# Kernel tuning notes

Hardware: AMD Instinct MI355X
Metric: run time of the kernel (lower is better)

Reference implementation:

```python
import jax, jax.numpy as jnp
import numpy as np

IN_DIM, UNITS, OUT_DIM = 128, 256, 8
DENSITY = 0.5  # 1 - sparsity_level
B, T = 256, 512


def _ncp_dims():
    Nm = OUT_DIM
    Nc = max(int(0.4 * (UNITS - Nm)), 1)   # command neurons (AutoNCP rule)
    Ni = UNITS - Nm - Nc                    # inter neurons
    return Ni, Nc, Nm


def _fanout_mask(rng, n_src, n_dst, fanout):
    # each source connects to `fanout` distinct random destinations
    idx = np.argsort(rng.random((n_src, n_dst)), axis=1)[:, :fanout]
    m = np.zeros((n_src, n_dst), dtype=np.int32)
    m[np.arange(n_src)[:, None], idx] = 1
    return m


def setup_inputs() -> dict:
    key = jax.random.key(0)
    rng = np.random.default_rng(22222)
    Ni, Nc, Nm = _ncp_dims()
    s_fan = max(int(Ni * DENSITY), 1)       # sensory fanout
    i_fan = max(int(Nc * DENSITY), 1)       # inter fanout
    m_fanin = max(int(Nc * DENSITY), 1)     # motor fanin
    M_si = _fanout_mask(rng, IN_DIM, Ni, s_fan)      # sensory -> inter
    M_ic = _fanout_mask(rng, Ni, Nc, i_fan)          # inter -> command
    M_cm = _fanout_mask(rng, Nm, Nc, m_fanin).T      # command -> motor (fanin per motor)

    def layer_mask(M_in, hid):
        # WiredCfCCell: concat input sparsity with dense ones for the recurrent block, then transpose
        return np.concatenate([M_in, np.ones((hid, hid), np.int32)], axis=0).T

    masks = [layer_mask(M_si, Ni), layer_mask(M_ic, Nc), layer_mask(M_cm, Nm)]
    dims = [(IN_DIM, Ni), (Ni, Nc), (Nc, Nm)]
    inp = {}
    for l, (fin, hid) in enumerate(dims):
        cat = fin + hid
        scale = 1.0 / np.sqrt(cat)
        for nm in ("w1", "w2", "wa", "wb"):
            inp[f"{nm}_{l}"] = jnp.asarray(rng.normal(0.0, scale, (hid, cat)).astype(np.float32))
        for nm in ("b1", "b2", "ba", "bb"):
            inp[f"{nm}_{l}"] = jnp.zeros((hid,), jnp.float32)
        inp[f"m{l}"] = jnp.asarray(masks[l])  # int32, constant sparsity mask
    k1, k2 = jax.random.split(key)
    inp["x"] = jax.random.normal(k1, (B, T, IN_DIM), jnp.float32)
    inp["dt"] = jax.random.uniform(k2, (1,), jnp.float32, 0.5, 1.5)
    return inp


def _cfc_cell(xh, w1, b1, w2, b2, wa, ba, wb, bb, m, ts):
    # CfCCell, mode='default', no backbone, sparsity mask on ff1/ff2 weights
    mf = m.astype(w1.dtype)
    ff1 = jnp.tanh(xh @ (w1 * mf).T + b1)
    ff2 = jnp.tanh(xh @ (w2 * mf).T + b2)
    t_interp = jax.nn.sigmoid((xh @ wa.T + ba) * ts + (xh @ wb.T + bb))
    return ff1 * (1.0 - t_interp) + t_interp * ff2


def _forward(x, dt, params, masks):
    Ni, Nc, Nm = _ncp_dims()
    ts = dt[0]
    h0 = jnp.zeros((x.shape[0], Ni), x.dtype)
    h1 = jnp.zeros((x.shape[0], Nc), x.dtype)
    h2 = jnp.zeros((x.shape[0], Nm), x.dtype)
    p0, p1, p2 = params

    def step(carry, xt):
        h0, h1, h2 = carry
        nh0 = _cfc_cell(jnp.concatenate([xt, h0], 1), *p0, masks[0], ts)
        nh1 = _cfc_cell(jnp.concatenate([nh0, h1], 1), *p1, masks[1], ts)
        nh2 = _cfc_cell(jnp.concatenate([nh1, h2], 1), *p2, masks[2], ts)
        return (nh0, nh1, nh2), nh2

    (h0, h1, h2), ys = jax.lax.scan(step, (h0, h1, h2), jnp.swapaxes(x, 0, 1))
    y = jnp.tanh(jnp.swapaxes(ys, 0, 1))          # (B, T, OUT_DIM), tanh output saturation
    h_out = jnp.concatenate([h0, h1, h2], axis=1)  # (B, units)
    return y, h_out


def reference(x, dt,
              w1_0, b1_0, w2_0, b2_0, wa_0, ba_0, wb_0, bb_0, m0,
              w1_1, b1_1, w2_1, b2_1, wa_1, ba_1, wb_1, bb_1, m1,
              w1_2, b1_2, w2_2, b2_2, wa_2, ba_2, wb_2, bb_2, m2):
    params = ((w1_0, b1_0, w2_0, b2_0, wa_0, ba_0, wb_0, bb_0),
              (w1_1, b1_1, w2_1, b2_1, wa_1, ba_1, wb_1, bb_1),
              (w1_2, b1_2, w2_2, b2_2, wa_2, ba_2, wb_2, bb_2))
    return _forward(x, dt, params, (m0, m1, m2))
```

## Files before the change

kernel.cpp:

```cpp
#include <hip/hip_runtime.h>
#include <cmath>


typedef _Float16 f16;
typedef f16 h4 __attribute__((ext_vector_type(4)));
typedef f16 h8 __attribute__((ext_vector_type(8)));
typedef float f4 __attribute__((ext_vector_type(4)));

#define MFMA(a, b, c) __builtin_amdgcn_mfma_f32_16x16x32_f16(a, b, c, 0, 0, 0)
#define RAW_BAR() asm volatile("s_waitcnt lgkmcnt(0)\n\ts_barrier" ::: "memory")

constexpr int IN_DIM = 128, Ni = 149, Nc = 99, Nm = 8;
constexpr int CAT0 = 277, CAT1 = 248, CAT2 = 107;
constexpr int Bsz = 256, Tsz = 512;
constexpr int TC = 64, NCH = 8, NBT = 16;
constexpr int NT0 = 30, NT1 = 21;
constexpr int S0 = 168, S2 = 136;
constexpr int NXWG1 = 64;
constexpr int NXWG0 = 128;
constexpr size_t XU0C = (size_t)TC * NBT * NT0 * 256;
constexpr size_t NH0C = (size_t)TC * NBT * 2560;
constexpr size_t XU1C = (size_t)TC * NBT * NT1 * 256;
constexpr size_t H0S_HALVES = (size_t)NBT * 16 * S0;
constexpr size_t H12S_HALVES = (size_t)NBT * 2 * 16 * S2;
constexpr size_t YOFF = (size_t)Bsz * Tsz * 8;

constexpr int OFF_X0 = 0;
constexpr int OFF_R0 = 7680;
constexpr int OFF_X1 = 17280;
constexpr int OFF_R12A = 24000;
constexpr int OFF_R12B = 29376;
constexpr int NFRAG = 30144;

__device__ inline float rcpf_(float x) { return __builtin_amdgcn_rcpf(x); }
__device__ __forceinline__ float cfc_h(float a0, float a1, float a2) {
  float e0 = __expf(a0), e1 = __expf(a1), e2 = __expf(a2);
  float pa = 1.f + e0, ma = 1.f - e0;
  float pb = 1.f + e1, mb = 1.f - e1;
  float pc = 1.f + e2;
  float num = fmaf(ma * pb, e2, mb * pa);
  return num * rcpf_(pa * pb * pc);
}
__device__ __forceinline__ float tanhp_(float x) {
  float e = __expf(-2.f * x);
  return (1.f - e) * rcpf_(1.f + e);
}

__global__ __launch_bounds__(256) void pack_kernel(
    const float* __restrict__ w1_0, const float* __restrict__ w2_0,
    const float* __restrict__ wa_0, const float* __restrict__ wb_0,
    const int* __restrict__ m0,
    const float* __restrict__ w1_1, const float* __restrict__ w2_1,
    const float* __restrict__ wa_1, const float* __restrict__ wb_1,
    const int* __restrict__ m1,
    const float* __restrict__ w1_2, const float* __restrict__ w2_2,
    const float* __restrict__ wa_2, const float* __restrict__ wb_2,
    const int* __restrict__ m2, const float* __restrict__ dtp,
    f16* __restrict__ PK) {
  int idx = blockIdx.x * 256 + threadIdx.x;
  if (idx >= NFRAG) return;
  int lane = idx & 63, col = lane & 15, q = lane >> 4;
  float ts = dtp[0];
  const float* Wa = nullptr;
  const float* Wb = nullptr;
  const int* M = nullptr;
  int ld, n, nmax, k0, kmax;
  int mat;
  if (idx < OFF_R0) {
    int p = idx >> 6;
    mat = p / 40; int nt = (p >> 2) % 10, kt = p & 3;
    ld = CAT0; n = nt * 16 + col; nmax = Ni; k0 = kt * 32 + q * 8; kmax = IN_DIM;
    if (mat == 0) { Wa = w1_0; M = m0; }
    else if (mat == 1) { Wa = w2_0; M = m0; }
    else { Wa = wa_0; Wb = wb_0; }
  } else if (idx < OFF_X1) {
    int p = (idx - OFF_R0) >> 6;
    int g = p / 15; mat = (p / 5) % 3; int kt = p % 5;
    ld = CAT0; n = g * 16 + col; nmax = Ni; k0 = IN_DIM + kt * 32 + q * 8; kmax = CAT0;
    if (mat == 0) Wa = w1_0;
    else if (mat == 1) Wa = w2_0;
    else { Wa = wa_0; Wb = wb_0; }
  } else if (idx < OFF_R12A) {
    int p = (idx - OFF_X1) >> 6;
    mat = p / 35; int nt = (p / 5) % 7, kt = p % 5;
    ld = CAT1; n = nt * 16 + col; nmax = Nc; k0 = kt * 32 + q * 8; kmax = Ni;
    if (mat == 0) { Wa = w1_1; M = m1; }
    else if (mat == 1) { Wa = w2_1; M = m1; }
    else { Wa = wa_1; Wb = wb_1; }
  } else if (idx < OFF_R12B) {
    int p = (idx - OFF_R12A) >> 6;
    int wv = p / 12; mat = (p / 4) % 3; int kt = p & 3;
    ld = CAT1; n = wv * 16 + col; nmax = Nc; k0 = Ni + kt * 32 + q * 8; kmax = CAT1;
    if (mat == 0) Wa = w1_1;
    else if (mat == 1) Wa = w2_1;
    else { Wa = wa_1; Wb = wb_1; }
  } else {
    int p = (idx - OFF_R12B) >> 6;
    mat = p / 4; int kt = p & 3;
    ld = CAT2; n = col; nmax = Nm; k0 = kt * 32 + q * 8; kmax = CAT2;
    if (mat == 0) { Wa = w1_2; M = m2; }
    else if (mat == 1) { Wa = w2_2; M = m2; }
    else { Wa = wa_2; Wb = wb_2; }
  }
  h8 r;
#pragma unroll
  for (int j = 0; j < 8; j++) {
    int k = k0 + j;
    float v = 0.f;
    if (n < nmax && k < kmax) {
      if (mat < 2) {
        v = Wa[(size_t)n * ld + k];
        if (M) v *= (float)M[(size_t)n * ld + k];
        v *= -2.f;
      } else {
        v = -(ts * Wa[(size_t)n * ld + k] + Wb[(size_t)n * ld + k]);
      }
    }
    r[j] = (f16)v;
  }
  ((h8*)PK)[idx] = r;
}

__device__ __forceinline__ void r0_step(
    const f16* br, f16* bw, const f16* __restrict__ XU0, f16* __restrict__ NH0,
    float* __restrict__ out, const h8 (&Bf)[3][5], h4 (&xu)[3],
    int t, int tload, int bt, int g, int lane, int col, int q, int n, bool last) {
  h8 A[5];
#pragma unroll
  for (int kt = 0; kt < 5; kt++)
    A[kt] = *(const h8*)(br + col * S0 + kt * 32 + q * 8);
  f4 acc0 = {(float)xu[0][0], (float)xu[0][1], (float)xu[0][2], (float)xu[0][3]};
  f4 acc1 = {(float)xu[1][0], (float)xu[1][1], (float)xu[1][2], (float)xu[1][3]};
  f4 acc2 = {(float)xu[2][0], (float)xu[2][1], (float)xu[2][2], (float)xu[2][3]};
  size_t mtl = (size_t)tload * NBT + bt;
#pragma unroll
  for (int mat = 0; mat < 3; mat++)
    xu[mat] = *(const h4*)(XU0 + (mtl * NT0 + mat * 10 + g) * 256 + lane * 4);
#pragma unroll
  for (int kt = 0; kt < 5; kt++) {
    acc0 = MFMA(A[kt], Bf[0][kt], acc0);
    acc1 = MFMA(A[kt], Bf[1][kt], acc1);
    acc2 = MFMA(A[kt], Bf[2][kt], acc2);
  }
  int mt = t * NBT + bt;
  f16* nh = NH0 + (size_t)mt * 2560;
#pragma unroll
  for (int r = 0; r < 4; r++) {
    int m = q * 4 + r;
    float h = cfc_h(acc0[r], acc1[r], acc2[r]);
    f16 h16 = (f16)h;
    bw[m * S0 + n] = h16;
    nh[m * 160 + n] = h16;
    if (last && n < Ni) out[YOFF + (size_t)(bt * 16 + m) * 256 + n] = h;
  }
}

__device__ __forceinline__ void r12l1_step(
    const f16* br, f16* bw, const f16* __restrict__ XU1, float* __restrict__ out,
    const h8 (&Bf)[3][4], h4 (&xu)[3],
    int tload, int bt, int w, int lane, int col, int q, int n, bool last) {
  h8 A[4];
#pragma unroll
  for (int kt = 0; kt < 4; kt++)
    A[kt] = *(const h8*)(br + col * S2 + kt * 32 + q * 8);
  f4 acc0 = {(float)xu[0][0], (float)xu[0][1], (float)xu[0][2], (float)xu[0][3]};
  f4 acc1 = {(float)xu[1][0], (float)xu[1][1], (float)xu[1][2], (float)xu[1][3]};
  f4 acc2 = {(float)xu[2][0], (float)xu[2][1], (float)xu[2][2], (float)xu[2][3]};
  size_t mtl = (size_t)tload * NBT + bt;
#pragma unroll
  for (int mat = 0; mat < 3; mat++)
    xu[mat] = *(const h4*)(XU1 + (mtl * NT1 + mat * 7 + w) * 256 + lane * 4);
#pragma unroll
  for (int kt = 0; kt < 4; kt++) {
    acc0 = MFMA(A[kt], Bf[0][kt], acc0);
    acc1 = MFMA(A[kt], Bf[1][kt], acc1);
    acc2 = MFMA(A[kt], Bf[2][kt], acc2);
  }
#pragma unroll
  for (int r = 0; r < 4; r++) {
    int m = q * 4 + r;
    float h = cfc_h(acc0[r], acc1[r], acc2[r]);
    if (n < Nc) {
      bw[m * S2 + n] = (f16)h;
      if (last) out[YOFF + (size_t)(bt * 16 + m) * 256 + Ni + n] = h;
    }
  }
}

__device__ __forceinline__ void r12l2_step(
    const f16* rb, f16* wb, float* __restrict__ out, const h8 (&Bf)[3][4],
    float bn0, float bn1, float bn2, int tg, int bt, int col, int q, bool last) {
  h8 A[4];
#pragma unroll
  for (int kt = 0; kt < 4; kt++)
    A[kt] = *(const h8*)(rb + col * S2 + kt * 32 + q * 8);
  f4 acc0 = {bn0, bn0, bn0, bn0};
  f4 acc1 = {bn1, bn1, bn1, bn1};
  f4 acc2 = {bn2, bn2, bn2, bn2};
#pragma unroll
  for (int kt = 0; kt < 4; kt++) {
    acc0 = MFMA(A[kt], Bf[0][kt], acc0);
    acc1 = MFMA(A[kt], Bf[1][kt], acc1);
    acc2 = MFMA(A[kt], Bf[2][kt], acc2);
  }
#pragma unroll
  for (int r = 0; r < 4; r++) {
    int m = q * 4 + r;
    float h = cfc_h(acc0[r], acc1[r], acc2[r]);
    if (col < Nm) {
      out[((size_t)(bt * 16 + m) * Tsz + tg) * 8 + col] = tanhp_(h);
      wb[m * S2 + Nc + col] = (f16)h;
      if (last) out[YOFF + (size_t)(bt * 16 + m) * 256 + Ni + Nc + col] = h;
    }
  }
}

__global__ __launch_bounds__(640) void R_kernel(
    const h8* __restrict__ pk,
    const float* __restrict__ b1_0, const float* __restrict__ b2_0,
    const float* __restrict__ ba_0, const float* __restrict__ bb_0,
    const float* __restrict__ b1_1, const float* __restrict__ b2_1,
    const float* __restrict__ ba_1, const float* __restrict__ bb_1,
    const float* __restrict__ c1, const float* __restrict__ c2,
    const float* __restrict__ ca, const float* __restrict__ cb,
    const float* __restrict__ dtp, const float* __restrict__ x,
    f16* __restrict__ XU0, f16* __restrict__ NH0, f16* __restrict__ XU1,
    f16* __restrict__ H0S, f16* __restrict__ H12S,
    float* __restrict__ out, int c) {
  __shared__ __align__(16) char smem[10752];
  int tid = threadIdx.x;
  int g = tid >> 6, lane = tid & 63, col = lane & 15, q = lane >> 4;
  int wg = blockIdx.x;
  float ts = dtp[0];

  if (wg < NBT) {
    if (c < 0 || c >= NCH) return;
    const f16* XU0r = XU0 + (size_t)(c & 1) * XU0C;
    f16* NH0w = NH0 + (size_t)(c & 1) * NH0C;
    f16(*buf)[16 * S0] = (f16(*)[16 * S0])smem;
    int bt = wg;
    int n = g * 16 + col;
    h8 Bf[3][5];
#pragma unroll
    for (int mat = 0; mat < 3; mat++)
#pragma unroll
      for (int kt = 0; kt < 5; kt++)
        Bf[mat][kt] = pk[OFF_R0 + ((g * 3 + mat) * 5 + kt) * 64 + lane];

    for (int idx = tid; idx < 16 * S0; idx += 640) {
      buf[0][idx] = (c == 0) ? (f16)0.f : H0S[(size_t)bt * 16 * S0 + idx];
      buf[1][idx] = (f16)0.f;
    }
    __syncthreads();

    h4 xu0[3], xu1[3], xu2[3], xu3[3];
#pragma unroll
    for (int mat = 0; mat < 3; mat++) {
      xu0[mat] = *(const h4*)(XU0r + ((size_t)(0 * NBT + bt) * NT0 + mat * 10 + g) * 256 + lane * 4);
      xu1[mat] = *(const h4*)(XU0r + ((size_t)(1 * NBT + bt) * NT0 + mat * 10 + g) * 256 + lane * 4);
      xu2[mat] = *(const h4*)(XU0r + ((size_t)(2 * NBT + bt) * NT0 + mat * 10 + g) * 256 + lane * 4);
      xu3[mat] = *(const h4*)(XU0r + ((size_t)(3 * NBT + bt) * NT0 + mat * 10 + g) * 256 + lane * 4);
    }

    for (int t = 0; t < TC; t += 4) {
      r0_step(buf[0], buf[1], XU0r, NH0w, out, Bf, xu0, t, (t + 4 < TC) ? t + 4 : t,
              bt, g, lane, col, q, n, false);
      RAW_BAR();
      r0_step(buf[1], buf[0], XU0r, NH0w, out, Bf, xu1, t + 1,
              (t + 5 < TC) ? t + 5 : t + 1, bt, g, lane, col, q, n, false);
      RAW_BAR();
      r0_step(buf[0], buf[1], XU0r, NH0w, out, Bf, xu2, t + 2,
              (t + 6 < TC) ? t + 6 : t + 2, bt, g, lane, col, q, n, false);
      RAW_BAR();
      bool lastD = (c == NCH - 1) && (t + 3 == TC - 1);
      r0_step(buf[1], buf[0], XU0r, NH0w, out, Bf, xu3, t + 3,
              (t + 7 < TC) ? t + 7 : t + 3, bt, g, lane, col, q, n, lastD);
      RAW_BAR();
    }
    for (int idx = tid; idx < 16 * S0; idx += 640)
      H0S[(size_t)bt * 16 * S0 + idx] = buf[0][idx];

  } else if (wg < 2 * NBT) {
    int cc = c - 2;
    if (cc < 0 || cc >= NCH) return;
    const f16* XU1r = XU1 + (size_t)(cc & 1) * XU1C;
    f16(*buf)[16 * S2] = (f16(*)[16 * S2])smem;
    int bt = wg - NBT;
    int w = g;
    int n = w * 16 + col;
    h8 Bf[3][4];
    float bn0 = 0.f, bn1 = 0.f, bn2 = 0.f;
    if (w < 7) {
#pragma unroll
      for (int mat = 0; mat < 3; mat++)
#pragma unroll
        for (int kt = 0; kt < 4; kt++)
          Bf[mat][kt] = pk[OFF_R12A + ((w * 3 + mat) * 4 + kt) * 64 + lane];
    } else if (w == 7) {
#pragma unroll
      for (int mat = 0; mat < 3; mat++)
#pragma unroll
        for (int kt = 0; kt < 4; kt++)
          Bf[mat][kt] = pk[OFF_R12B + (mat * 4 + kt) * 64 + lane];
      bn0 = (col < Nm) ? -2.f * c1[col] : 0.f;
      bn1 = (col < Nm) ? -2.f * c2[col] : 0.f;
      bn2 = (col < Nm) ? -(ts * ca[col] + cb[col]) : 0.f;
    }
    for (int idx = tid; idx < 2 * 16 * S2; idx += 640)
      ((f16*)buf)[idx] = (cc == 0) ? (f16)0.f : H12S[(size_t)bt * 2 * 16 * S2 + idx];
    __syncthreads();

    h4 xuA[3], xuB[3];
    if (w < 7) {
#pragma unroll
      for (int mat = 0; mat < 3; mat++) {
        xuA[mat] = *(const h4*)(XU1r + ((size_t)bt * NT1 + mat * 7 + w) * 256 + lane * 4);
        xuB[mat] = *(const h4*)(XU1r +
                                ((size_t)(NBT + bt) * NT1 + mat * 7 + w) * 256 + lane * 4);
      }
    }

    for (int t = 0; t < TC; t += 2) {
      if (w < 7) {
        int tlA = (t + 2 < TC) ? t + 2 : t;
        r12l1_step(buf[0], buf[1], XU1r, out, Bf, xuA, tlA, bt, w, lane, col, q, n,
                   false);
      }
      RAW_BAR();
      if (w == 7)
        r12l2_step(buf[1], buf[0], out, Bf, bn0, bn1, bn2, cc * TC + t, bt, col, q,
                   false);
      if (w < 7) {
        int tlB = (t + 3 < TC) ? t + 3 : t + 1;
        bool lastB = (cc == NCH - 1) && (t + 1 == TC - 1);
        r12l1_step(buf[1], buf[0], XU1r, out, Bf, xuB, tlB, bt, w, lane, col, q, n,
                   lastB);
      }
      RAW_BAR();
      if (w == 7)
        r12l2_step(buf[0], buf[1], out, Bf, bn0, bn1, bn2, cc * TC + t + 1, bt, col, q,
                   (cc == NCH - 1) && (t + 1 == TC - 1));
    }
    __syncthreads();
    for (int idx = tid; idx < 2 * 16 * S2; idx += 640)
      H12S[(size_t)bt * 2 * 16 * S2 + idx] = ((f16*)buf)[idx];

  } else if (wg < 2 * NBT + NXWG1) {
    int cx = c - 1;
    if (cx < 0 || cx >= NCH) return;
    int w = g;
    if (w >= 7) return;
    const f16* NH0r = NH0 + (size_t)(cx & 1) * NH0C;
    f16* XU1w = XU1 + (size_t)(cx & 1) * XU1C;
    int bx = wg - 2 * NBT;
    int n = w * 16 + col;
    h8 Bf[3][5];
    float bias[3];
#pragma unroll
    for (int mat = 0; mat < 3; mat++)
#pragma unroll
      for (int kt = 0; kt < 5; kt++)
        Bf[mat][kt] = pk[OFF_X1 + (mat * 35 + w * 5 + kt) * 64 + lane];
    bias[0] = (n < Nc) ? -2.f * b1_1[n] : 0.f;
    bias[1] = (n < Nc) ? -2.f * b2_1[n] : 0.f;
    bias[2] = (n < Nc) ? -(ts * ba_1[n] + bb_1[n]) : 0.f;
    for (int i = 0; i < (TC * NBT) / NXWG1; i++) {
      int mt = bx * ((TC * NBT) / NXWG1) + i;
      const f16* Ab = NH0r + (size_t)mt * 2560;
      h8 A[5];
#pragma unroll
      for (int kt = 0; kt < 5; kt++)
        A[kt] = *(const h8*)(Ab + col * 160 + kt * 32 + q * 8);
#pragma unroll
      for (int mat = 0; mat < 3; mat++) {
        float b = bias[mat];
        f4 acc = {b, b, b, b};
#pragma unroll
        for (int kt = 0; kt < 5; kt++) acc = MFMA(A[kt], Bf[mat][kt], acc);
        h4 o;
#pragma unroll
        for (int rr = 0; rr < 4; rr++) o[rr] = (f16)acc[rr];
        *(h4*)(XU1w + ((size_t)mt * NT1 + mat * 7 + w) * 256 + lane * 4) = o;
      }
    }

  } else {
    int cn = c + 1;
    if (cn >= NCH) return;
    f16* XU0w = XU0 + (size_t)(cn & 1) * XU0C;
    f16* stg = (f16*)smem;
    int bx = wg - 2 * NBT - NXWG1;
    int w = g;
    int n = w * 16 + col;
    h8 Bx[3][4];
    float bias[3];
#pragma unroll
    for (int mat = 0; mat < 3; mat++)
#pragma unroll
      for (int kt = 0; kt < 4; kt++)
        Bx[mat][kt] = pk[OFF_X0 + ((mat * 10 + w) * 4 + kt) * 64 + lane];
    bias[0] = (n < Ni) ? -2.f * b1_0[n] : 0.f;
    bias[1] = (n < Ni) ? -2.f * b2_0[n] : 0.f;
    bias[2] = (n < Ni) ? -(ts * ba_0[n] + bb_0[n]) : 0.f;
    for (int i = 0; i < (TC * NBT) / NXWG0; i++) {
      int mt = bx * ((TC * NBT) / NXWG0) + i;
      int tl = mt >> 4, bt = mt & 15;
      int tg = cn * TC + tl;
      if (tid < 256) {
        int sr = tid >> 4, sc = (tid & 15) * 8;
        const float* xp = x + ((size_t)(bt * 16 + sr) * Tsz + tg) * IN_DIM + sc;
        h8 hv;
#pragma unroll
        for (int j = 0; j < 8; j++) hv[j] = (f16)xp[j];
        *(h8*)(stg + sr * 136 + sc) = hv;
      }
      __syncthreads();
      h8 A[4];
#pragma unroll
      for (int kt = 0; kt < 4; kt++)
        A[kt] = *(const h8*)(stg + col * 136 + kt * 32 + q * 8);
#pragma unroll
      for (int mat = 0; mat < 3; mat++) {
        float b = bias[mat];
        f4 acc = {b, b, b, b};
#pragma unroll
        for (int kt = 0; kt < 4; kt++) acc = MFMA(A[kt], Bx[mat][kt], acc);
        h4 o;
#pragma unroll
        for (int rr = 0; rr < 4; rr++) o[rr] = (f16)acc[rr];
        *(h4*)(XU0w + ((size_t)mt * NT0 + mat * 10 + w) * 256 + lane * 4) = o;
      }
      __syncthreads();
    }
  }
}

extern "C" void kernel_launch(void* const* d_in, const int* in_sizes, int n_in,
                              void* d_out, int out_size, void* d_ws, size_t ws_size,
                              hipStream_t stream) {
  const float* w1_0 = (const float*)d_in[0];
  const float* w2_0 = (const float*)d_in[1];
  const float* wa_0 = (const float*)d_in[2];
  const float* wb_0 = (const float*)d_in[3];
  const float* b1_0 = (const float*)d_in[4];
  const float* b2_0 = (const float*)d_in[5];
  const float* ba_0 = (const float*)d_in[6];
  const float* bb_0 = (const float*)d_in[7];
  const int* m0 = (const int*)d_in[8];
  const float* w1_1 = (const float*)d_in[9];
  const float* w2_1 = (const float*)d_in[10];
  const float* wa_1 = (const float*)d_in[11];
  const float* wb_1 = (const float*)d_in[12];
  const float* b1_1 = (const float*)d_in[13];
  const float* b2_1 = (const float*)d_in[14];
  const float* ba_1 = (const float*)d_in[15];
  const float* bb_1 = (const float*)d_in[16];
  const int* m1 = (const int*)d_in[17];
  const float* w1_2 = (const float*)d_in[18];
  const float* w2_2 = (const float*)d_in[19];
  const float* wa_2 = (const float*)d_in[20];
  const float* wb_2 = (const float*)d_in[21];
  const float* c1 = (const float*)d_in[22];
  const float* c2 = (const float*)d_in[23];
  const float* ca = (const float*)d_in[24];
  const float* cb = (const float*)d_in[25];
  const int* m2 = (const int*)d_in[26];
  const float* x = (const float*)d_in[27];
  const float* dt = (const float*)d_in[28];
  float* out = (float*)d_out;

  f16* XU0 = (f16*)d_ws;
  f16* NH0 = XU0 + 2 * XU0C;
  f16* XU1 = NH0 + 2 * NH0C;
  f16* H0S = XU1 + 2 * XU1C;
  f16* H12S = H0S + H0S_HALVES;
  f16* PK = H12S + H12S_HALVES;
  const h8* pk = (const h8*)PK;

  pack_kernel<<<(NFRAG + 255) / 256, 256, 0, stream>>>(
      w1_0, w2_0, wa_0, wb_0, m0, w1_1, w2_1, wa_1, wb_1, m1,
      w1_2, w2_2, wa_2, wb_2, m2, dt, PK);

  for (int c = -1; c <= NCH + 1; c++)
    R_kernel<<<2 * NBT + NXWG1 + NXWG0, 640, 0, stream>>>(
        pk, b1_0, b2_0, ba_0, bb_0, b1_1, b2_1, ba_1, bb_1,
        c1, c2, ca, cb, dt, x, XU0, NH0, XU1, H0S, H12S, out, c);
}
```

Baseline: 772.7 us.

## Fuse layer-1 input projection into recurrent stage and use exp2 scaling

Removes the separate XU1 projection stage (NH0 times layer-1 input weights) and computes it inside the layer-1/2 recurrent workgroups, reading NH0 directly with a prefetch of the next timestep's A fragments. This drops one pipeline stage, so there is one fewer kernel launch and no XU1 workspace round trip. In exchange the serial recurrent step takes 15 more MFMAs and holds more registers. All pre-activations are also folded by log2(e) so the nonlinearities can use hardware exp2 instead of __expf, and launch bounds now ask for one block per CU.

```diff
diff --git a/kernel.cpp b/kernel.cpp
--- a/kernel.cpp
+++ b/kernel.cpp
@@ -14,16 +14,15 @@
 constexpr int CAT0 = 277, CAT1 = 248, CAT2 = 107;
 constexpr int Bsz = 256, Tsz = 512;
 constexpr int TC = 64, NCH = 8, NBT = 16;
-constexpr int NT0 = 30, NT1 = 21;
+constexpr int NT0 = 30;
 constexpr int S0 = 168, S2 = 136;
-constexpr int NXWG1 = 64;
 constexpr int NXWG0 = 128;
 constexpr size_t XU0C = (size_t)TC * NBT * NT0 * 256;
 constexpr size_t NH0C = (size_t)TC * NBT * 2560;
-constexpr size_t XU1C = (size_t)TC * NBT * NT1 * 256;
 constexpr size_t H0S_HALVES = (size_t)NBT * 16 * S0;
 constexpr size_t H12S_HALVES = (size_t)NBT * 2 * 16 * S2;
 constexpr size_t YOFF = (size_t)Bsz * Tsz * 8;
+constexpr float L2E = 1.4426950408889634f;
 
 constexpr int OFF_X0 = 0;
 constexpr int OFF_R0 = 7680;
@@ -33,8 +32,15 @@
 constexpr int NFRAG = 30144;
 
 __device__ inline float rcpf_(float x) { return __builtin_amdgcn_rcpf(x); }
+__device__ __forceinline__ float exp2p_(float x) {
+#if __has_builtin(__builtin_amdgcn_exp2f)
+  return __builtin_amdgcn_exp2f(x);
+#else
+  return exp2f(x);
+#endif
+}
 __device__ __forceinline__ float cfc_h(float a0, float a1, float a2) {
-  float e0 = __expf(a0), e1 = __expf(a1), e2 = __expf(a2);
+  float e0 = exp2p_(a0), e1 = exp2p_(a1), e2 = exp2p_(a2);
   float pa = 1.f + e0, ma = 1.f - e0;
   float pb = 1.f + e1, mb = 1.f - e1;
   float pc = 1.f + e2;
@@ -42,7 +48,7 @@
   return num * rcpf_(pa * pb * pc);
 }
 __device__ __forceinline__ float tanhp_(float x) {
-  float e = __expf(-2.f * x);
+  float e = exp2p_(-2.f * L2E * x);
   return (1.f - e) * rcpf_(1.f + e);
 }
 
@@ -111,9 +117,9 @@
       if (mat < 2) {
         v = Wa[(size_t)n * ld + k];
         if (M) v *= (float)M[(size_t)n * ld + k];
-        v *= -2.f;
+        v *= -2.f * L2E;
       } else {
-        v = -(ts * Wa[(size_t)n * ld + k] + Wb[(size_t)n * ld + k]);
+        v = -L2E * (ts * Wa[(size_t)n * ld + k] + Wb[(size_t)n * ld + k]);
       }
     }
     r[j] = (f16)v;
@@ -156,26 +162,33 @@
 }
 
 __device__ __forceinline__ void r12l1_step(
-    const f16* br, f16* bw, const f16* __restrict__ XU1, float* __restrict__ out,
-    const h8 (&Bf)[3][4], h4 (&xu)[3],
-    int tload, int bt, int w, int lane, int col, int q, int n, bool last) {
-  h8 A[4];
+    const f16* br, f16* bw, const f16* __restrict__ NH0r, float* __restrict__ out,
+    const h8 (&BfI)[3][5], const h8 (&BfR)[3][4], h8 (&A)[5],
+    float bn0, float bn1, float bn2,
+    int tload, int bt, int col, int q, int n, bool last) {
+  h8 Ar[4];
 #pragma unroll
   for (int kt = 0; kt < 4; kt++)
-    A[kt] = *(const h8*)(br + col * S2 + kt * 32 + q * 8);
-  f4 acc0 = {(float)xu[0][0], (float)xu[0][1], (float)xu[0][2], (float)xu[0][3]};
-  f4 acc1 = {(float)xu[1][0], (float)xu[1][1], (float)xu[1][2], (float)xu[1][3]};
-  f4 acc2 = {(float)xu[2][0], (float)xu[2][1], (float)xu[2][2], (float)xu[2][3]};
-  size_t mtl = (size_t)tload * NBT + bt;
-#pragma unroll
-  for (int mat = 0; mat < 3; mat++)
-    xu[mat] = *(const h4*)(XU1 + (mtl * NT1 + mat * 7 + w) * 256 + lane * 4);
+    Ar[kt] = *(const h8*)(br + col * S2 + kt * 32 + q * 8);
+  f4 acc0 = {bn0, bn0, bn0, bn0};
+  f4 acc1 = {bn1, bn1, bn1, bn1};
+  f4 acc2 = {bn2, bn2, bn2, bn2};
+#pragma unroll
+  for (int kt = 0; kt < 5; kt++) {
+    acc0 = MFMA(A[kt], BfI[0][kt], acc0);
+    acc1 = MFMA(A[kt], BfI[1][kt], acc1);
+    acc2 = MFMA(A[kt], BfI[2][kt], acc2);
+  }
 #pragma unroll
   for (int kt = 0; kt < 4; kt++) {
-    acc0 = MFMA(A[kt], Bf[0][kt], acc0);
-    acc1 = MFMA(A[kt], Bf[1][kt], acc1);
-    acc2 = MFMA(A[kt], Bf[2][kt], acc2);
-  }
+    acc0 = MFMA(Ar[kt], BfR[0][kt], acc0);
+    acc1 = MFMA(Ar[kt], BfR[1][kt], acc1);
+    acc2 = MFMA(Ar[kt], BfR[2][kt], acc2);
+  }
+  const f16* Ab = NH0r + ((size_t)tload * NBT + bt) * 2560;
+#pragma unroll
+  for (int kt = 0; kt < 5; kt++)
+    A[kt] = *(const h8*)(Ab + col * 160 + kt * 32 + q * 8);
 #pragma unroll
   for (int r = 0; r < 4; r++) {
     int m = q * 4 + r;
@@ -215,7 +228,7 @@
   }
 }
 
-__global__ __launch_bounds__(640) void R_kernel(
+__global__ __launch_bounds__(640, 1) void R_kernel(
     const h8* __restrict__ pk,
     const float* __restrict__ b1_0, const float* __restrict__ b2_0,
     const float* __restrict__ ba_0, const float* __restrict__ bb_0,
@@ -224,7 +237,7 @@
     const float* __restrict__ c1, const float* __restrict__ c2,
     const float* __restrict__ ca, const float* __restrict__ cb,
     const float* __restrict__ dtp, const float* __restrict__ x,
-    f16* __restrict__ XU0, f16* __restrict__ NH0, f16* __restrict__ XU1,
+    f16* __restrict__ XU0, f16* __restrict__ NH0,
     f16* __restrict__ H0S, f16* __restrict__ H12S,
     float* __restrict__ out, int c) {
   __shared__ __align__(16) char smem[10752];
@@ -281,115 +294,81 @@
       H0S[(size_t)bt * 16 * S0 + idx] = buf[0][idx];
 
   } else if (wg < 2 * NBT) {
-    int cc = c - 2;
+    int cc = c - 1;
     if (cc < 0 || cc >= NCH) return;
-    const f16* XU1r = XU1 + (size_t)(cc & 1) * XU1C;
+    const f16* NH0r = NH0 + (size_t)(cc & 1) * NH0C;
     f16(*buf)[16 * S2] = (f16(*)[16 * S2])smem;
     int bt = wg - NBT;
     int w = g;
     int n = w * 16 + col;
-    h8 Bf[3][4];
+    h8 BfI[3][5];
+    h8 BfR[3][4];
     float bn0 = 0.f, bn1 = 0.f, bn2 = 0.f;
     if (w < 7) {
 #pragma unroll
+      for (int mat = 0; mat < 3; mat++) {
+#pragma unroll
+        for (int kt = 0; kt < 5; kt++)
+          BfI[mat][kt] = pk[OFF_X1 + (mat * 35 + w * 5 + kt) * 64 + lane];
+#pragma unroll
+        for (int kt = 0; kt < 4; kt++)
+          BfR[mat][kt] = pk[OFF_R12A + ((w * 3 + mat) * 4 + kt) * 64 + lane];
+      }
+      bn0 = (n < Nc) ? -2.f * L2E * b1_1[n] : 0.f;
+      bn1 = (n < Nc) ? -2.f * L2E * b2_1[n] : 0.f;
+      bn2 = (n < Nc) ? -L2E * (ts * ba_1[n] + bb_1[n]) : 0.f;
+    } else if (w == 7) {
+#pragma unroll
       for (int mat = 0; mat < 3; mat++)
 #pragma unroll
         for (int kt = 0; kt < 4; kt++)
-          Bf[mat][kt] = pk[OFF_R12A + ((w * 3 + mat) * 4 + kt) * 64 + lane];
-    } else if (w == 7) {
-#pragma unroll
-      for (int mat = 0; mat < 3; mat++)
-#pragma unroll
-        for (int kt = 0; kt < 4; kt++)
-          Bf[mat][kt] = pk[OFF_R12B + (mat * 4 + kt) * 64 + lane];
-      bn0 = (col < Nm) ? -2.f * c1[col] : 0.f;
-      bn1 = (col < Nm) ? -2.f * c2[col] : 0.f;
-      bn2 = (col < Nm) ? -(ts * ca[col] + cb[col]) : 0.f;
+          BfR[mat][kt] = pk[OFF_R12B + (mat * 4 + kt) * 64 + lane];
+      bn0 = (col < Nm) ? -2.f * L2E * c1[col] : 0.f;
+      bn1 = (col < Nm) ? -2.f * L2E * c2[col] : 0.f;
+      bn2 = (col < Nm) ? -L2E * (ts * ca[col] + cb[col]) : 0.f;
+    }
+    h8 Aa[5], Ab[5];
+    if (w < 7) {
+      const f16* A0 = NH0r + (size_t)(0 * NBT + bt) * 2560;
+      const f16* A1 = NH0r + (size_t)(1 * NBT + bt) * 2560;
+#pragma unroll
+      for (int kt = 0; kt < 5; kt++) {
+        Aa[kt] = *(const h8*)(A0 + col * 160 + kt * 32 + q * 8);
+        Ab[kt] = *(const h8*)(A1 + col * 160 + kt * 32 + q * 8);
+      }
     }
     for (int idx = tid; idx < 2 * 16 * S2; idx += 640)
       ((f16*)buf)[idx] = (cc == 0) ? (f16)0.f : H12S[(size_t)bt * 2 * 16 * S2 + idx];
     __syncthreads();
 
-    h4 xuA[3], xuB[3];
-    if (w < 7) {
-#pragma unroll
-      for (int mat = 0; mat < 3; mat++) {
-        xuA[mat] = *(const h4*)(XU1r + ((size_t)bt * NT1 + mat * 7 + w) * 256 + lane * 4);
-        xuB[mat] = *(const h4*)(XU1r +
-                                ((size_t)(NBT + bt) * NT1 + mat * 7 + w) * 256 + lane * 4);
-      }
-    }
-
     for (int t = 0; t < TC; t += 2) {
-      if (w < 7) {
-        int tlA = (t + 2 < TC) ? t + 2 : t;
-        r12l1_step(buf[0], buf[1], XU1r, out, Bf, xuA, tlA, bt, w, lane, col, q, n,
-                   false);
-      }
+      if (w < 7)
+        r12l1_step(buf[0], buf[1], NH0r, out, BfI, BfR, Aa, bn0, bn1, bn2,
+                   (t + 2 < TC) ? t + 2 : t, bt, col, q, n, false);
       RAW_BAR();
       if (w == 7)
-        r12l2_step(buf[1], buf[0], out, Bf, bn0, bn1, bn2, cc * TC + t, bt, col, q,
+        r12l2_step(buf[1], buf[0], out, BfR, bn0, bn1, bn2, cc * TC + t, bt, col, q,
                    false);
       if (w < 7) {
-        int tlB = (t + 3 < TC) ? t + 3 : t + 1;
         bool lastB = (cc == NCH - 1) && (t + 1 == TC - 1);
-        r12l1_step(buf[1], buf[0], XU1r, out, Bf, xuB, tlB, bt, w, lane, col, q, n,
-                   lastB);
+        r12l1_step(buf[1], buf[0], NH0r, out, BfI, BfR, Ab, bn0, bn1, bn2,
+                   (t + 3 < TC) ? t + 3 : t + 1, bt, col, q, n, lastB);
       }
       RAW_BAR();
       if (w == 7)
-        r12l2_step(buf[0], buf[1], out, Bf, bn0, bn1, bn2, cc * TC + t + 1, bt, col, q,
+        r12l2_step(buf[0], buf[1], out, BfR, bn0, bn1, bn2, cc * TC + t + 1, bt, col, q,
                    (cc == NCH - 1) && (t + 1 == TC - 1));
     }
     __syncthreads();
     for (int idx = tid; idx < 2 * 16 * S2; idx += 640)
       H12S[(size_t)bt * 2 * 16 * S2 + idx] = ((f16*)buf)[idx];
-
-  } else if (wg < 2 * NBT + NXWG1) {
-    int cx = c - 1;
-    if (cx < 0 || cx >= NCH) return;
-    int w = g;
-    if (w >= 7) return;
-    const f16* NH0r = NH0 + (size_t)(cx & 1) * NH0C;
-    f16* XU1w = XU1 + (size_t)(cx & 1) * XU1C;
-    int bx = wg - 2 * NBT;
-    int n = w * 16 + col;
-    h8 Bf[3][5];
-    float bias[3];
-#pragma unroll
-    for (int mat = 0; mat < 3; mat++)
-#pragma unroll
-      for (int kt = 0; kt < 5; kt++)
-        Bf[mat][kt] = pk[OFF_X1 + (mat * 35 + w * 5 + kt) * 64 + lane];
-    bias[0] = (n < Nc) ? -2.f * b1_1[n] : 0.f;
-    bias[1] = (n < Nc) ? -2.f * b2_1[n] : 0.f;
-    bias[2] = (n < Nc) ? -(ts * ba_1[n] + bb_1[n]) : 0.f;
-    for (int i = 0; i < (TC * NBT) / NXWG1; i++) {
-      int mt = bx * ((TC * NBT) / NXWG1) + i;
-      const f16* Ab = NH0r + (size_t)mt * 2560;
-      h8 A[5];
-#pragma unroll
-      for (int kt = 0; kt < 5; kt++)
-        A[kt] = *(const h8*)(Ab + col * 160 + kt * 32 + q * 8);
-#pragma unroll
-      for (int mat = 0; mat < 3; mat++) {
-        float b = bias[mat];
-        f4 acc = {b, b, b, b};
-#pragma unroll
-        for (int kt = 0; kt < 5; kt++) acc = MFMA(A[kt], Bf[mat][kt], acc);
-        h4 o;
-#pragma unroll
-        for (int rr = 0; rr < 4; rr++) o[rr] = (f16)acc[rr];
-        *(h4*)(XU1w + ((size_t)mt * NT1 + mat * 7 + w) * 256 + lane * 4) = o;
-      }
-    }
 
   } else {
     int cn = c + 1;
     if (cn >= NCH) return;
     f16* XU0w = XU0 + (size_t)(cn & 1) * XU0C;
     f16* stg = (f16*)smem;
-    int bx = wg - 2 * NBT - NXWG1;
+    int bx = wg - 2 * NBT;
     int w = g;
     int n = w * 16 + col;
     h8 Bx[3][4];
@@ -399,9 +378,9 @@
 #pragma unroll
       for (int kt = 0; kt < 4; kt++)
         Bx[mat][kt] = pk[OFF_X0 + ((mat * 10 + w) * 4 + kt) * 64 + lane];
-    bias[0] = (n < Ni) ? -2.f * b1_0[n] : 0.f;
-    bias[1] = (n < Ni) ? -2.f * b2_0[n] : 0.f;
-    bias[2] = (n < Ni) ? -(ts * ba_0[n] + bb_0[n]) : 0.f;
+    bias[0] = (n < Ni) ? -2.f * L2E * b1_0[n] : 0.f;
+    bias[1] = (n < Ni) ? -2.f * L2E * b2_0[n] : 0.f;
+    bias[2] = (n < Ni) ? -L2E * (ts * ba_0[n] + bb_0[n]) : 0.f;
     for (int i = 0; i < (TC * NBT) / NXWG0; i++) {
       int mt = bx * ((TC * NBT) / NXWG0) + i;
       int tl = mt >> 4, bt = mt & 15;
@@ -471,8 +450,7 @@
 
   f16* XU0 = (f16*)d_ws;
   f16* NH0 = XU0 + 2 * XU0C;
-  f16* XU1 = NH0 + 2 * NH0C;
-  f16* H0S = XU1 + 2 * XU1C;
+  f16* H0S = NH0 + 2 * NH0C;
   f16* H12S = H0S + H0S_HALVES;
   f16* PK = H12S + H12S_HALVES;
   const h8* pk = (const h8*)PK;
@@ -481,8 +459,8 @@
       w1_0, w2_0, wa_0, wb_0, m0, w1_1, w2_1, wa_1, wb_1, m1,
       w1_2, w2_2, wa_2, wb_2, m2, dt, PK);
 
-  for (int c = -1; c <= NCH + 1; c++)
-    R_kernel<<<2 * NBT + NXWG1 + NXWG0, 640, 0, stream>>>(
+  for (int c = -1; c <= NCH; c++)
+    R_kernel<<<2 * NBT + NXWG0, 640, 0, stream>>>(
         pk, b1_0, b2_0, ba_0, bb_0, b1_1, b2_1, ba_1, bb_1,
-        c1, c2, ca, cb, dt, x, XU0, NH0, XU1, H0S, H12S, out, c);
-}
+        c1, c2, ca, cb, dt, x, XU0, NH0, H0S, H12S, out, c);
+}
```

After: 1.620 ms. 110% more time.

## Fuse pack and chunked phase launches into one persistent cooperative kernel

Applied to the files above, without the earlier changes.

The weight-pack kernel and the eleven per-chunk launches of the pipelined recurrent kernel are merged into a single cooperative launch that uses grid.sync between phases. Recurrent state now stays in LDS across chunks instead of being spilled to and reloaded from global scratch. The exponentials are switched to exp2, with log2(e) folded into the packed weights and biases. This removes per-launch overhead and the state save and restore, at the cost of grid-wide barriers and a requirement that all 240 workgroups be co-resident.

```diff
diff --git a/kernel.cpp b/kernel.cpp
--- a/kernel.cpp
+++ b/kernel.cpp
@@ -1,6 +1,9 @@
 #include <hip/hip_runtime.h>
+#include <hip/hip_cooperative_groups.h>
 #include <cmath>
 
+
+namespace cg = cooperative_groups;
 
 typedef _Float16 f16;
 typedef f16 h4 __attribute__((ext_vector_type(4)));
@@ -18,12 +21,12 @@
 constexpr int S0 = 168, S2 = 136;
 constexpr int NXWG1 = 64;
 constexpr int NXWG0 = 128;
+constexpr int NWG = 2 * NBT + NXWG1 + NXWG0;
 constexpr size_t XU0C = (size_t)TC * NBT * NT0 * 256;
 constexpr size_t NH0C = (size_t)TC * NBT * 2560;
 constexpr size_t XU1C = (size_t)TC * NBT * NT1 * 256;
-constexpr size_t H0S_HALVES = (size_t)NBT * 16 * S0;
-constexpr size_t H12S_HALVES = (size_t)NBT * 2 * 16 * S2;
 constexpr size_t YOFF = (size_t)Bsz * Tsz * 8;
+constexpr float L2E = 1.4426950408889634f;
 
 constexpr int OFF_X0 = 0;
 constexpr int OFF_R0 = 7680;
@@ -33,8 +36,15 @@
 constexpr int NFRAG = 30144;
 
 __device__ inline float rcpf_(float x) { return __builtin_amdgcn_rcpf(x); }
+__device__ __forceinline__ float exp2p_(float x) {
+#if __has_builtin(__builtin_amdgcn_exp2f)
+  return __builtin_amdgcn_exp2f(x);
+#else
+  return exp2f(x);
+#endif
+}
 __device__ __forceinline__ float cfc_h(float a0, float a1, float a2) {
-  float e0 = __expf(a0), e1 = __expf(a1), e2 = __expf(a2);
+  float e0 = exp2p_(a0), e1 = exp2p_(a1), e2 = exp2p_(a2);
   float pa = 1.f + e0, ma = 1.f - e0;
   float pb = 1.f + e1, mb = 1.f - e1;
   float pc = 1.f + e2;
@@ -42,11 +52,12 @@
   return num * rcpf_(pa * pb * pc);
 }
 __device__ __forceinline__ float tanhp_(float x) {
-  float e = __expf(-2.f * x);
+  float e = exp2p_(-2.f * L2E * x);
   return (1.f - e) * rcpf_(1.f + e);
 }
 
-__global__ __launch_bounds__(256) void pack_kernel(
+__device__ __forceinline__ void pack_one(
+    int idx,
     const float* __restrict__ w1_0, const float* __restrict__ w2_0,
     const float* __restrict__ wa_0, const float* __restrict__ wb_0,
     const int* __restrict__ m0,
@@ -55,12 +66,8 @@
     const int* __restrict__ m1,
     const float* __restrict__ w1_2, const float* __restrict__ w2_2,
     const float* __restrict__ wa_2, const float* __restrict__ wb_2,
-    const int* __restrict__ m2, const float* __restrict__ dtp,
-    f16* __restrict__ PK) {
-  int idx = blockIdx.x * 256 + threadIdx.x;
-  if (idx >= NFRAG) return;
+    const int* __restrict__ m2, float ts, f16* __restrict__ PK) {
   int lane = idx & 63, col = lane & 15, q = lane >> 4;
-  float ts = dtp[0];
   const float* Wa = nullptr;
   const float* Wb = nullptr;
   const int* M = nullptr;
@@ -111,9 +118,9 @@
       if (mat < 2) {
         v = Wa[(size_t)n * ld + k];
         if (M) v *= (float)M[(size_t)n * ld + k];
-        v *= -2.f;
+        v *= -2.f * L2E;
       } else {
-        v = -(ts * Wa[(size_t)n * ld + k] + Wb[(size_t)n * ld + k]);
+        v = -L2E * (ts * Wa[(size_t)n * ld + k] + Wb[(size_t)n * ld + k]);
       }
     }
     r[j] = (f16)v;
@@ -215,28 +222,43 @@
   }
 }
 
-__global__ __launch_bounds__(640) void R_kernel(
-    const h8* __restrict__ pk,
+__global__ __launch_bounds__(640) void cfc_kernel(
+    f16* __restrict__ PK,
+    const float* __restrict__ w1_0, const float* __restrict__ w2_0,
+    const float* __restrict__ wa_0, const float* __restrict__ wb_0,
+    const int* __restrict__ m0,
     const float* __restrict__ b1_0, const float* __restrict__ b2_0,
     const float* __restrict__ ba_0, const float* __restrict__ bb_0,
+    const float* __restrict__ w1_1, const float* __restrict__ w2_1,
+    const float* __restrict__ wa_1, const float* __restrict__ wb_1,
+    const int* __restrict__ m1,
     const float* __restrict__ b1_1, const float* __restrict__ b2_1,
     const float* __restrict__ ba_1, const float* __restrict__ bb_1,
+    const float* __restrict__ w1_2, const float* __restrict__ w2_2,
+    const float* __restrict__ wa_2, const float* __restrict__ wb_2,
+    const int* __restrict__ m2,
     const float* __restrict__ c1, const float* __restrict__ c2,
     const float* __restrict__ ca, const float* __restrict__ cb,
     const float* __restrict__ dtp, const float* __restrict__ x,
     f16* __restrict__ XU0, f16* __restrict__ NH0, f16* __restrict__ XU1,
-    f16* __restrict__ H0S, f16* __restrict__ H12S,
-    float* __restrict__ out, int c) {
+    float* __restrict__ out) {
   __shared__ __align__(16) char smem[10752];
+  cg::grid_group grid = cg::this_grid();
   int tid = threadIdx.x;
   int g = tid >> 6, lane = tid & 63, col = lane & 15, q = lane >> 4;
   int wg = blockIdx.x;
   float ts = dtp[0];
+  const h8* pk = (const h8*)PK;
+
+  {
+    int gtid = wg * 640 + tid;
+    if (gtid < NFRAG)
+      pack_one(gtid, w1_0, w2_0, wa_0, wb_0, m0, w1_1, w2_1, wa_1, wb_1, m1,
+               w1_2, w2_2, wa_2, wb_2, m2, ts, PK);
+  }
+  grid.sync();
 
   if (wg < NBT) {
-    if (c < 0 || c >= NCH) return;
-    const f16* XU0r = XU0 + (size_t)(c & 1) * XU0C;
-    f16* NH0w = NH0 + (size_t)(c & 1) * NH0C;
     f16(*buf)[16 * S0] = (f16(*)[16 * S0])smem;
     int bt = wg;
     int n = g * 16 + col;
@@ -246,44 +268,42 @@
 #pragma unroll
       for (int kt = 0; kt < 5; kt++)
         Bf[mat][kt] = pk[OFF_R0 + ((g * 3 + mat) * 5 + kt) * 64 + lane];
-
-    for (int idx = tid; idx < 16 * S0; idx += 640) {
-      buf[0][idx] = (c == 0) ? (f16)0.f : H0S[(size_t)bt * 16 * S0 + idx];
-      buf[1][idx] = (f16)0.f;
-    }
+    for (int idx = tid; idx < 2 * 16 * S0; idx += 640) ((f16*)buf)[idx] = (f16)0.f;
     __syncthreads();
 
-    h4 xu0[3], xu1[3], xu2[3], xu3[3];
-#pragma unroll
-    for (int mat = 0; mat < 3; mat++) {
-      xu0[mat] = *(const h4*)(XU0r + ((size_t)(0 * NBT + bt) * NT0 + mat * 10 + g) * 256 + lane * 4);
-      xu1[mat] = *(const h4*)(XU0r + ((size_t)(1 * NBT + bt) * NT0 + mat * 10 + g) * 256 + lane * 4);
-      xu2[mat] = *(const h4*)(XU0r + ((size_t)(2 * NBT + bt) * NT0 + mat * 10 + g) * 256 + lane * 4);
-      xu3[mat] = *(const h4*)(XU0r + ((size_t)(3 * NBT + bt) * NT0 + mat * 10 + g) * 256 + lane * 4);
-    }
-
-    for (int t = 0; t < TC; t += 4) {
-      r0_step(buf[0], buf[1], XU0r, NH0w, out, Bf, xu0, t, (t + 4 < TC) ? t + 4 : t,
-              bt, g, lane, col, q, n, false);
-      RAW_BAR();
-      r0_step(buf[1], buf[0], XU0r, NH0w, out, Bf, xu1, t + 1,
-              (t + 5 < TC) ? t + 5 : t + 1, bt, g, lane, col, q, n, false);
-      RAW_BAR();
-      r0_step(buf[0], buf[1], XU0r, NH0w, out, Bf, xu2, t + 2,
-              (t + 6 < TC) ? t + 6 : t + 2, bt, g, lane, col, q, n, false);
-      RAW_BAR();
-      bool lastD = (c == NCH - 1) && (t + 3 == TC - 1);
-      r0_step(buf[1], buf[0], XU0r, NH0w, out, Bf, xu3, t + 3,
-              (t + 7 < TC) ? t + 7 : t + 3, bt, g, lane, col, q, n, lastD);
-      RAW_BAR();
-    }
-    for (int idx = tid; idx < 16 * S0; idx += 640)
-      H0S[(size_t)bt * 16 * S0 + idx] = buf[0][idx];
+    for (int ph = -1; ph <= NCH + 1; ++ph) {
+      if (ph >= 0 && ph < NCH) {
+        int c = ph;
+        const f16* XU0r = XU0 + (size_t)(c & 1) * XU0C;
+        f16* NH0w = NH0 + (size_t)(c & 1) * NH0C;
+        h4 xu0[3], xu1[3], xu2[3], xu3[3];
+#pragma unroll
+        for (int mat = 0; mat < 3; mat++) {
+          xu0[mat] = *(const h4*)(XU0r + ((size_t)(0 * NBT + bt) * NT0 + mat * 10 + g) * 256 + lane * 4);
+          xu1[mat] = *(const h4*)(XU0r + ((size_t)(1 * NBT + bt) * NT0 + mat * 10 + g) * 256 + lane * 4);
+          xu2[mat] = *(const h4*)(XU0r + ((size_t)(2 * NBT + bt) * NT0 + mat * 10 + g) * 256 + lane * 4);
+          xu3[mat] = *(const h4*)(XU0r + ((size_t)(3 * NBT + bt) * NT0 + mat * 10 + g) * 256 + lane * 4);
+        }
+        for (int t = 0; t < TC; t += 4) {
+          r0_step(buf[0], buf[1], XU0r, NH0w, out, Bf, xu0, t,
+                  (t + 4 < TC) ? t + 4 : t, bt, g, lane, col, q, n, false);
+          RAW_BAR();
+          r0_step(buf[1], buf[0], XU0r, NH0w, out, Bf, xu1, t + 1,
+                  (t + 5 < TC) ? t + 5 : t + 1, bt, g, lane, col, q, n, false);
+          RAW_BAR();
+          r0_step(buf[0], buf[1], XU0r, NH0w, out, Bf, xu2, t + 2,
+                  (t + 6 < TC) ? t + 6 : t + 2, bt, g, lane, col, q, n, false);
+          RAW_BAR();
+          bool lastD = (c == NCH - 1) && (t + 3 == TC - 1);
+          r0_step(buf[1], buf[0], XU0r, NH0w, out, Bf, xu3, t + 3,
+                  (t + 7 < TC) ? t + 7 : t + 3, bt, g, lane, col, q, n, lastD);
+          RAW_BAR();
+        }
+      }
+      if (ph <= NCH) grid.sync();
+    }
 
   } else if (wg < 2 * NBT) {
-    int cc = c - 2;
-    if (cc < 0 || cc >= NCH) return;
-    const f16* XU1r = XU1 + (size_t)(cc & 1) * XU1C;
     f16(*buf)[16 * S2] = (f16(*)[16 * S2])smem;
     int bt = wg - NBT;
     int w = g;
@@ -302,92 +322,96 @@
 #pragma unroll
         for (int kt = 0; kt < 4; kt++)
           Bf[mat][kt] = pk[OFF_R12B + (mat * 4 + kt) * 64 + lane];
-      bn0 = (col < Nm) ? -2.f * c1[col] : 0.f;
-      bn1 = (col < Nm) ? -2.f * c2[col] : 0.f;
-      bn2 = (col < Nm) ? -(ts * ca[col] + cb[col]) : 0.f;
-    }
-    for (int idx = tid; idx < 2 * 16 * S2; idx += 640)
-      ((f16*)buf)[idx] = (cc == 0) ? (f16)0.f : H12S[(size_t)bt * 2 * 16 * S2 + idx];
+      bn0 = (col < Nm) ? -2.f * L2E * c1[col] : 0.f;
+      bn1 = (col < Nm) ? -2.f * L2E * c2[col] : 0.f;
+      bn2 = (col < Nm) ? -L2E * (ts * ca[col] + cb[col]) : 0.f;
+    }
+    for (int idx = tid; idx < 2 * 16 * S2; idx += 640) ((f16*)buf)[idx] = (f16)0.f;
     __syncthreads();
 
-    h4 xuA[3], xuB[3];
-    if (w < 7) {
-#pragma unroll
-      for (int mat = 0; mat < 3; mat++) {
-        xuA[mat] = *(const h4*)(XU1r + ((size_t)bt * NT1 + mat * 7 + w) * 256 + lane * 4);
-        xuB[mat] = *(const h4*)(XU1r +
-                                ((size_t)(NBT + bt) * NT1 + mat * 7 + w) * 256 + lane * 4);
+    for (int ph = -1; ph <= NCH + 1; ++ph) {
+      int cc = ph - 2;
+      if (cc >= 0 && cc < NCH) {
+        const f16* XU1r = XU1 + (size_t)(cc & 1) * XU1C;
+        h4 xuA[3], xuB[3];
+        if (w < 7) {
+#pragma unroll
+          for (int mat = 0; mat < 3; mat++) {
+            xuA[mat] = *(const h4*)(XU1r + ((size_t)bt * NT1 + mat * 7 + w) * 256 + lane * 4);
+            xuB[mat] = *(const h4*)(XU1r +
+                                    ((size_t)(NBT + bt) * NT1 + mat * 7 + w) * 256 + lane * 4);
+          }
+        }
+        for (int t = 0; t < TC; t += 2) {
+          if (w < 7) {
+            int tlA = (t + 2 < TC) ? t + 2 : t;
+            r12l1_step(buf[0], buf[1], XU1r, out, Bf, xuA, tlA, bt, w, lane, col, q,
+                       n, false);
+          }
+          RAW_BAR();
+          if (w == 7)
+            r12l2_step(buf[1], buf[0], out, Bf, bn0, bn1, bn2, cc * TC + t, bt, col,
+                       q, false);
+          if (w < 7) {
+            int tlB = (t + 3 < TC) ? t + 3 : t + 1;
+            bool lastB = (cc == NCH - 1) && (t + 1 == TC - 1);
+            r12l1_step(buf[1], buf[0], XU1r, out, Bf, xuB, tlB, bt, w, lane, col, q,
+                       n, lastB);
+          }
+          RAW_BAR();
+          if (w == 7)
+            r12l2_step(buf[0], buf[1], out, Bf, bn0, bn1, bn2, cc * TC + t + 1, bt,
+                       col, q, (cc == NCH - 1) && (t + 1 == TC - 1));
+        }
       }
-    }
-
-    for (int t = 0; t < TC; t += 2) {
-      if (w < 7) {
-        int tlA = (t + 2 < TC) ? t + 2 : t;
-        r12l1_step(buf[0], buf[1], XU1r, out, Bf, xuA, tlA, bt, w, lane, col, q, n,
-                   false);
-      }
-      RAW_BAR();
-      if (w == 7)
-        r12l2_step(buf[1], buf[0], out, Bf, bn0, bn1, bn2, cc * TC + t, bt, col, q,
-                   false);
-      if (w < 7) {
-        int tlB = (t + 3 < TC) ? t + 3 : t + 1;
-        bool lastB = (cc == NCH - 1) && (t + 1 == TC - 1);
-        r12l1_step(buf[1], buf[0], XU1r, out, Bf, xuB, tlB, bt, w, lane, col, q, n,
-                   lastB);
-      }
-      RAW_BAR();
-      if (w == 7)
-        r12l2_step(buf[0], buf[1], out, Bf, bn0, bn1, bn2, cc * TC + t + 1, bt, col, q,
-                   (cc == NCH - 1) && (t + 1 == TC - 1));
-    }
-    __syncthreads();
-    for (int idx = tid; idx < 2 * 16 * S2; idx += 640)
-      H12S[(size_t)bt * 2 * 16 * S2 + idx] = ((f16*)buf)[idx];
+      if (ph <= NCH) grid.sync();
+    }
 
   } else if (wg < 2 * NBT + NXWG1) {
-    int cx = c - 1;
-    if (cx < 0 || cx >= NCH) return;
+    int bx = wg - 2 * NBT;
     int w = g;
-    if (w >= 7) return;
-    const f16* NH0r = NH0 + (size_t)(cx & 1) * NH0C;
-    f16* XU1w = XU1 + (size_t)(cx & 1) * XU1C;
-    int bx = wg - 2 * NBT;
     int n = w * 16 + col;
     h8 Bf[3][5];
-    float bias[3];
-#pragma unroll
-    for (int mat = 0; mat < 3; mat++)
-#pragma unroll
-      for (int kt = 0; kt < 5; kt++)
-        Bf[mat][kt] = pk[OFF_X1 + (mat * 35 + w * 5 + kt) * 64 + lane];
-    bias[0] = (n < Nc) ? -2.f * b1_1[n] : 0.f;
-    bias[1] = (n < Nc) ? -2.f * b2_1[n] : 0.f;
-    bias[2] = (n < Nc) ? -(ts * ba_1[n] + bb_1[n]) : 0.f;
-    for (int i = 0; i < (TC * NBT) / NXWG1; i++) {
-      int mt = bx * ((TC * NBT) / NXWG1) + i;
-      const f16* Ab = NH0r + (size_t)mt * 2560;
-      h8 A[5];
-#pragma unroll
-      for (int kt = 0; kt < 5; kt++)
-        A[kt] = *(const h8*)(Ab + col * 160 + kt * 32 + q * 8);
-#pragma unroll
-      for (int mat = 0; mat < 3; mat++) {
-        float b = bias[mat];
-        f4 acc = {b, b, b, b};
-#pragma unroll
-        for (int kt = 0; kt < 5; kt++) acc = MFMA(A[kt], Bf[mat][kt], acc);
-        h4 o;
-#pragma unroll
-        for (int rr = 0; rr < 4; rr++) o[rr] = (f16)acc[rr];
-        *(h4*)(XU1w + ((size_t)mt * NT1 + mat * 7 + w) * 256 + lane * 4) = o;
+    float bias[3] = {0.f, 0.f, 0.f};
+    if (w < 7) {
+#pragma unroll
+      for (int mat = 0; mat < 3; mat++)
+#pragma unroll
+        for (int kt = 0; kt < 5; kt++)
+          Bf[mat][kt] = pk[OFF_X1 + (mat * 35 + w * 5 + kt) * 64 + lane];
+      bias[0] = (n < Nc) ? -2.f * L2E * b1_1[n] : 0.f;
+      bias[1] = (n < Nc) ? -2.f * L2E * b2_1[n] : 0.f;
+      bias[2] = (n < Nc) ? -L2E * (ts * ba_1[n] + bb_1[n]) : 0.f;
+    }
+    for (int ph = -1; ph <= NCH + 1; ++ph) {
+      int cx = ph - 1;
+      if (w < 7 && cx >= 0 && cx < NCH) {
+        const f16* NH0r = NH0 + (size_t)(cx & 1) * NH0C;
+        f16* XU1w = XU1 + (size_t)(cx & 1) * XU1C;
+        for (int i = 0; i < (TC * NBT) / NXWG1; i++) {
+          int mt = bx * ((TC * NBT) / NXWG1) + i;
+          const f16* Ab = NH0r + (size_t)mt * 2560;
+          h8 A[5];
+#pragma unroll
+          for (int kt = 0; kt < 5; kt++)
+            A[kt] = *(const h8*)(Ab + col * 160 + kt * 32 + q * 8);
+#pragma unroll
+          for (int mat = 0; mat < 3; mat++) {
+            float b = bias[mat];
+            f4 acc = {b, b, b, b};
+#pragma unroll
+            for (int kt = 0; kt < 5; kt++) acc = MFMA(A[kt], Bf[mat][kt], acc);
+            h4 o;
+#pragma unroll
+            for (int rr = 0; rr < 4; rr++) o[rr] = (f16)acc[rr];
+            *(h4*)(XU1w + ((size_t)mt * NT1 + mat * 7 + w) * 256 + lane * 4) = o;
+          }
+        }
       }
+      if (ph <= NCH) grid.sync();
     }
 
   } else {
-    int cn = c + 1;
-    if (cn >= NCH) return;
-    f16* XU0w = XU0 + (size_t)(cn & 1) * XU0C;
     f16* stg = (f16*)smem;
     int bx = wg - 2 * NBT - NXWG1;
     int w = g;
@@ -399,38 +423,45 @@
 #pragma unroll
       for (int kt = 0; kt < 4; kt++)
         Bx[mat][kt] = pk[OFF_X0 + ((mat * 10 + w) * 4 + kt) * 64 + lane];
-    bias[0] = (n < Ni) ? -2.f * b1_0[n] : 0.f;
-    bias[1] = (n < Ni) ? -2.f * b2_0[n] : 0.f;
-    bias[2] = (n < Ni) ? -(ts * ba_0[n] + bb_0[n]) : 0.f;
-    for (int i = 0; i < (TC * NBT) / NXWG0; i++) {
-      int mt = bx * ((TC * NBT) / NXWG0) + i;
-      int tl = mt >> 4, bt = mt & 15;
-      int tg = cn * TC + tl;
-      if (tid < 256) {
-        int sr = tid >> 4, sc = (tid & 15) * 8;
-        const float* xp = x + ((size_t)(bt * 16 + sr) * Tsz + tg) * IN_DIM + sc;
-        h8 hv;
-#pragma unroll
-        for (int j = 0; j < 8; j++) hv[j] = (f16)xp[j];
-        *(h8*)(stg + sr * 136 + sc) = hv;
+    bias[0] = (n < Ni) ? -2.f * L2E * b1_0[n] : 0.f;
+    bias[1] = (n < Ni) ? -2.f * L2E * b2_0[n] : 0.f;
+    bias[2] = (n < Ni) ? -L2E * (ts * ba_0[n] + bb_0[n]) : 0.f;
+    for (int ph = -1; ph <= NCH + 1; ++ph) {
+      int cn = ph + 1;
+      if (cn >= 0 && cn < NCH) {
+        f16* XU0w = XU0 + (size_t)(cn & 1) * XU0C;
+        for (int i = 0; i < (TC * NBT) / NXWG0; i++) {
+          int mt = bx * ((TC * NBT) / NXWG0) + i;
+          int tl = mt >> 4, bt = mt & 15;
+          int tg = cn * TC + tl;
+          if (tid < 256) {
+            int sr = tid >> 4, sc = (tid & 15) * 8;
+            const float* xp = x + ((size_t)(bt * 16 + sr) * Tsz + tg) * IN_DIM + sc;
+            h8 hv;
+#pragma unroll
+            for (int j = 0; j < 8; j++) hv[j] = (f16)xp[j];
+            *(h8*)(stg + sr * 136 + sc) = hv;
+          }
+          __syncthreads();
+          h8 A[4];
+#pragma unroll
+          for (int kt = 0; kt < 4; kt++)
+            A[kt] = *(const h8*)(stg + col * 136 + kt * 32 + q * 8);
+#pragma unroll
+          for (int mat = 0; mat < 3; mat++) {
+            float b = bias[mat];
+            f4 acc = {b, b, b, b};
+#pragma unroll
+            for (int kt = 0; kt < 4; kt++) acc = MFMA(A[kt], Bx[mat][kt], acc);
+            h4 o;
+#pragma unroll
+            for (int rr = 0; rr < 4; rr++) o[rr] = (f16)acc[rr];
+            *(h4*)(XU0w + ((size_t)mt * NT0 + mat * 10 + w) * 256 + lane * 4) = o;
+          }
+          __syncthreads();
+        }
       }
-      __syncthreads();
-      h8 A[4];
-#pragma unroll
-      for (int kt = 0; kt < 4; kt++)
-        A[kt] = *(const h8*)(stg + col * 136 + kt * 32 + q * 8);
-#pragma unroll
-      for (int mat = 0; mat < 3; mat++) {
-        float b = bias[mat];
-        f4 acc = {b, b, b, b};
-#pragma unroll
-        for (int kt = 0; kt < 4; kt++) acc = MFMA(A[kt], Bx[mat][kt], acc);
-        h4 o;
-#pragma unroll
-        for (int rr = 0; rr < 4; rr++) o[rr] = (f16)acc[rr];
-        *(h4*)(XU0w + ((size_t)mt * NT0 + mat * 10 + w) * 256 + lane * 4) = o;
-      }
-      __syncthreads();
+      if (ph <= NCH) grid.sync();
     }
   }
 }
@@ -472,17 +503,17 @@
   f16* XU0 = (f16*)d_ws;
   f16* NH0 = XU0 + 2 * XU0C;
   f16* XU1 = NH0 + 2 * NH0C;
-  f16* H0S = XU1 + 2 * XU1C;
-  f16* H12S = H0S + H0S_HALVES;
-  f16* PK = H12S + H12S_HALVES;
-  const h8* pk = (const h8*)PK;
-
-  pack_kernel<<<(NFRAG + 255) / 256, 256, 0, stream>>>(
-      w1_0, w2_0, wa_0, wb_0, m0, w1_1, w2_1, wa_1, wb_1, m1,
-      w1_2, w2_2, wa_2, wb_2, m2, dt, PK);
-
-  for (int c = -1; c <= NCH + 1; c++)
-    R_kernel<<<2 * NBT + NXWG1 + NXWG0, 640, 0, stream>>>(
-        pk, b1_0, b2_0, ba_0, bb_0, b1_1, b2_1, ba_1, bb_1,
-        c1, c2, ca, cb, dt, x, XU0, NH0, XU1, H0S, H12S, out, c);
-}
+  f16* PK = XU1 + 2 * XU1C;
+
+  void* args[] = {
+      &PK,
+      &w1_0, &w2_0, &wa_0, &wb_0, &m0, &b1_0, &b2_0, &ba_0, &bb_0,
+      &w1_1, &w2_1, &wa_1, &wb_1, &m1, &b1_1, &b2_1, &ba_1, &bb_1,
+      &w1_2, &w2_2, &wa_2, &wb_2, &m2,
+      &c1, &c2, &ca, &cb,
+      &dt, &x,
+      &XU0, &NH0, &XU1,
+      &out};
+  hipLaunchCooperativeKernel((void*)cfc_kernel, dim3(NWG), dim3(640), args, 0,
+                             stream);
+}
```

New measurement: 1.004 ms. 30.0% more time.
